# Kernel optimization log

Hardware: AMD Instinct MI355X
Metric: run time of the kernel (lower is better)

## Reference

```python
import jax, jax.numpy as jnp
import numpy as np
import math

D_MODEL = 1024
HEADS = 16
D_K = D_MODEL // HEADS
BATCH = 4
SEQ = 1024


def setup_inputs() -> dict:
    key = jax.random.key(0)
    ks = jax.random.split(key, 12)
    s = 1.0 / math.sqrt(D_MODEL)
    inp = {
        "q": jax.random.normal(ks[0], (BATCH, SEQ, D_MODEL), jnp.float32),
        "k": jax.random.normal(ks[1], (BATCH, SEQ, D_MODEL), jnp.float32),
        "v": jax.random.normal(ks[2], (BATCH, SEQ, D_MODEL), jnp.float32),
        # causal mask, broadcastable over (batch, heads)
        "mask": jnp.tril(jnp.ones((SEQ, SEQ), jnp.bool_))[None, None, :, :],
        "Wq": jax.random.normal(ks[3], (D_MODEL, D_MODEL), jnp.float32) * s,
        "bq": jax.random.normal(ks[4], (D_MODEL,), jnp.float32) * 0.01,
        "Wk": jax.random.normal(ks[5], (D_MODEL, D_MODEL), jnp.float32) * s,
        "bk": jax.random.normal(ks[6], (D_MODEL,), jnp.float32) * 0.01,
        "Wv": jax.random.normal(ks[7], (D_MODEL, D_MODEL), jnp.float32) * s,
        "bv": jax.random.normal(ks[8], (D_MODEL,), jnp.float32) * 0.01,
        "Wo": jax.random.normal(ks[9], (D_MODEL, D_MODEL), jnp.float32) * s,
        "bo": jax.random.normal(ks[10], (D_MODEL,), jnp.float32) * 0.01,
    }
    return inp


def reference(q, k, v, mask, Wq, bq, Wk, bk, Wv, bv, Wo, bo):
    B, S, _ = q.shape
    # projections (torch Linear: x @ W.T + b; here W stored as [in, out])
    def proj(x, W, b):
        return (x @ W + b).reshape(B, -1, HEADS, D_K).transpose(0, 2, 1, 3)

    Q = proj(q, Wq, bq)  # [B, H, S, Dk]
    K = proj(k, Wk, bk)
    V = proj(v, Wv, bv)

    scores = jnp.einsum("bhqd,bhkd->bhqk", Q, K) / math.sqrt(D_K)
    scores = jnp.where(mask, scores, jnp.float32(-1e9))
    attn = jax.nn.softmax(scores, axis=-1)  # dropout p=0.0 -> identity
    x = jnp.einsum("bhqk,bhkd->bhqd", attn, V)
    x = x.transpose(0, 2, 1, 3).reshape(B, S, D_MODEL)
    return x @ Wo + bo
```

## Files before the change

### kernel.cpp

```cpp
#include <hip/hip_runtime.h>
#include <math.h>

typedef __bf16 bf16_t;
typedef bf16_t bf16x8 __attribute__((ext_vector_type(8)));
typedef bf16_t bf16x4 __attribute__((ext_vector_type(4)));
typedef float  floatx4 __attribute__((ext_vector_type(4)));
typedef unsigned int u32;

#define MFMA_BF16(a, b, c) __builtin_amdgcn_mfma_f32_16x16x32_bf16((a), (b), (c), 0, 0, 0)

static constexpr int DMODEL = 1024;
static constexpr int NHEAD  = 16;
static constexpr int HDIM   = 64;
static constexpr int NBATCH = 4;
static constexpr int SEQLEN = 1024;
static constexpr int NTOK   = NBATCH * SEQLEN;

typedef __attribute__((address_space(3))) void       as3_void;
typedef __attribute__((address_space(1))) const void as1_cvoid;

__device__ __forceinline__ void gload16(const void* g, void* l) {
    __builtin_amdgcn_global_load_lds((as1_cvoid*)g, (as3_void*)l, 16, 0, 0);
}

__device__ __forceinline__ bf16x8 load_cvt8(const float* __restrict__ p) {
    floatx4 a = *(const floatx4*)p;
    floatx4 b = *(const floatx4*)(p + 4);
    bf16x8 r;
    r[0] = (bf16_t)a[0]; r[1] = (bf16_t)a[1]; r[2] = (bf16_t)a[2]; r[3] = (bf16_t)a[3];
    r[4] = (bf16_t)b[0]; r[5] = (bf16_t)b[1]; r[6] = (bf16_t)b[2]; r[7] = (bf16_t)b[3];
    return r;
}

__global__ __launch_bounds__(256) void prep(
    const float* __restrict__ W0, const float* __restrict__ W1,
    const float* __restrict__ W2, const float* __restrict__ W3,
    const float* __restrict__ q, const float* __restrict__ k, const float* __restrict__ v,
    bf16_t* __restrict__ Wt, bf16_t* __restrict__ Xr)
{
    __shared__ float tile[32][33];
    const int z = blockIdx.z;
    if (z < 4) {
        const float* W = (z == 0) ? W0 : (z == 1) ? W1 : (z == 2) ? W2 : W3;
        bf16_t* O = Wt + (size_t)z * DMODEL * DMODEL;
        const int tx = threadIdx.x & 31, ty = threadIdx.x >> 5;
        const int r0 = blockIdx.x * 32, c0 = blockIdx.y * 32;
#pragma unroll
        for (int i = 0; i < 32; i += 8)
            tile[ty + i][tx] = W[(size_t)(r0 + ty + i) * DMODEL + c0 + tx];
        __syncthreads();
#pragma unroll
        for (int i = 0; i < 32; i += 8)
            O[(size_t)(c0 + ty + i) * DMODEL + r0 + tx] = (bf16_t)tile[tx][ty + i];
    } else {
        const float* src = (z == 4) ? q : (z == 5) ? k : v;
        bf16_t* dst = Xr + (size_t)(z - 4) * ((size_t)NTOK * DMODEL);
        size_t i = (((size_t)blockIdx.y * 32 + blockIdx.x) * 256 + threadIdx.x) * 16;
        *(bf16x8*)(dst + i)     = load_cvt8(src + i);
        *(bf16x8*)(dst + i + 8) = load_cvt8(src + i + 8);
    }
}

__global__ __launch_bounds__(256) void transpose_w(
    const float* __restrict__ W0, const float* __restrict__ W1,
    const float* __restrict__ W2, const float* __restrict__ W3,
    bf16_t* __restrict__ out)
{
    __shared__ float tile[32][33];
    const float* W = (blockIdx.z == 0) ? W0 : (blockIdx.z == 1) ? W1
                   : (blockIdx.z == 2) ? W2 : W3;
    bf16_t* O = out + (size_t)blockIdx.z * DMODEL * DMODEL;
    int tx = threadIdx.x, ty = threadIdx.y;
    int r0 = blockIdx.x * 32, c0 = blockIdx.y * 32;
#pragma unroll
    for (int i = 0; i < 32; i += 8)
        tile[ty + i][tx] = W[(size_t)(r0 + ty + i) * DMODEL + c0 + tx];
    __syncthreads();
#pragma unroll
    for (int i = 0; i < 32; i += 8)
        O[(size_t)(c0 + ty + i) * DMODEL + r0 + tx] = (bf16_t)tile[tx][ty + i];
}
__global__ __launch_bounds__(256) void cvt_bf16(
    const float* __restrict__ src, bf16_t* __restrict__ dst)
{
    size_t i = ((size_t)blockIdx.x * 256 + threadIdx.x) * 8;
    *(bf16x8*)(dst + i) = load_cvt8(src + i);
}

__global__ __launch_bounds__(256) void gemm_qkv(
    const bf16_t* __restrict__ Xb, size_t astride, int mode0,
    const bf16_t* __restrict__ Wt,
    const float* __restrict__ bq, const float* __restrict__ bk, const float* __restrict__ bv,
    bf16_t* __restrict__ Qh, bf16_t* __restrict__ Kh, bf16_t* __restrict__ Vt)
{
    const int mode = mode0 + blockIdx.z;
    const bf16_t* A = Xb + astride * (size_t)blockIdx.z;
    const bf16_t* B = Wt + (size_t)mode * DMODEL * DMODEL;
    const float* bias = (mode == 0) ? bq : (mode == 1) ? bk : bv;
    bf16_t* out       = (mode == 0) ? Qh : (mode == 1) ? Kh : Vt;

    __shared__ __align__(16) bf16_t lA[2][128 * 32];
    __shared__ __align__(16) bf16_t lB[2][128 * 32];

    const int wave = threadIdx.x >> 6, lane = threadIdx.x & 63;
    const int quad = lane >> 4, l15 = lane & 15;
    const int wm = wave >> 1, wn = wave & 1;
    const int row0 = blockIdx.x * 128, col0 = blockIdx.y * 128;
    const int srow = lane >> 2, scol = (lane & 3) * 8;

    const floatx4 zero = {0.f, 0.f, 0.f, 0.f};
    floatx4 acc[4][4];
#pragma unroll
    for (int mt = 0; mt < 4; mt++)
#pragma unroll
        for (int nt = 0; nt < 4; nt++) acc[mt][nt] = zero;

#pragma unroll
    for (int j = 0; j < 2; j++) {
        const int seg = j * 4 + wave;
        gload16(A + (size_t)(row0 + seg * 16 + srow) * DMODEL + scol, lA[0] + seg * 512);
        gload16(B + (size_t)(col0 + seg * 16 + srow) * DMODEL + scol, lB[0] + seg * 512);
    }

    for (int it = 0; it < 32; it++) {
        __syncthreads();
        const int cur = it & 1;
        if (it + 1 < 32) {
            const int k1 = (it + 1) * 32;
            const int nb = cur ^ 1;
#pragma unroll
            for (int j = 0; j < 2; j++) {
                const int seg = j * 4 + wave;
                gload16(A + (size_t)(row0 + seg * 16 + srow) * DMODEL + k1 + scol, lA[nb] + seg * 512);
                gload16(B + (size_t)(col0 + seg * 16 + srow) * DMODEL + k1 + scol, lB[nb] + seg * 512);
            }
        }
        bf16x8 aF[4], bF[4];
#pragma unroll
        for (int t = 0; t < 4; t++) {
            aF[t] = *(const bf16x8*)(lA[cur] + (wm * 64 + t * 16 + l15) * 32 + quad * 8);
            bF[t] = *(const bf16x8*)(lB[cur] + (wn * 64 + t * 16 + l15) * 32 + quad * 8);
        }
#pragma unroll
        for (int mt = 0; mt < 4; mt++)
#pragma unroll
            for (int nt = 0; nt < 4; nt++)
                acc[mt][nt] = MFMA_BF16(aF[mt], bF[nt], acc[mt][nt]);
    }

#pragma unroll
    for (int nt = 0; nt < 4; nt++) {
        const int gn = col0 + wn * 64 + nt * 16 + l15;
        const float bb = bias[gn];
        const int hh = gn >> 6, dd = gn & 63;
#pragma unroll
        for (int mt = 0; mt < 4; mt++) {
#pragma unroll
            for (int r = 0; r < 4; r++) {
                const int tok = row0 + wm * 64 + mt * 16 + quad * 4 + r;
                const int b = tok >> 10, s = tok & 1023;
                float vv = acc[mt][nt][r] + bb;
                size_t addr;
                if (mode == 2) {
                    addr = ((size_t)((b * NHEAD + hh) * HDIM + dd)) * SEQLEN + s;
                } else {
                    if (mode == 0) vv *= 0.125f;
                    addr = ((size_t)((b * NHEAD + hh) * SEQLEN + s)) * HDIM + dd;
                }
                out[addr] = (bf16_t)vv;
            }
        }
    }
}

__global__ __launch_bounds__(256) void gemm_o(
    const bf16_t* __restrict__ Xa, const bf16_t* __restrict__ Wt,
    const float* __restrict__ bias, float* __restrict__ out)
{
    __shared__ __align__(16) bf16_t lA[2][64 * 32];
    __shared__ __align__(16) bf16_t lB[2][128 * 32];

    const int wave = threadIdx.x >> 6, lane = threadIdx.x & 63;
    const int quad = lane >> 4, l15 = lane & 15;
    const int wm = wave & 1, wn = wave >> 1;
    const int row0 = blockIdx.x * 64, col0 = blockIdx.y * 128;
    const int srow = lane >> 2, scol = (lane & 3) * 8;

    const floatx4 zero = {0.f, 0.f, 0.f, 0.f};
    floatx4 acc[2][4];
#pragma unroll
    for (int mt = 0; mt < 2; mt++)
#pragma unroll
        for (int nt = 0; nt < 4; nt++) acc[mt][nt] = zero;

    gload16(Xa + (size_t)(row0 + wave * 16 + srow) * DMODEL + scol, lA[0] + wave * 512);
#pragma unroll
    for (int j = 0; j < 2; j++) {
        const int seg = wave * 2 + j;
        gload16(Wt + (size_t)(col0 + seg * 16 + srow) * DMODEL + scol, lB[0] + seg * 512);
    }

    for (int it = 0; it < 32; it++) {
        __syncthreads();
        const int cur = it & 1;
        if (it + 1 < 32) {
            const int k1 = (it + 1) * 32;
            const int nb = cur ^ 1;
            gload16(Xa + (size_t)(row0 + wave * 16 + srow) * DMODEL + k1 + scol, lA[nb] + wave * 512);
#pragma unroll
            for (int j = 0; j < 2; j++) {
                const int seg = wave * 2 + j;
                gload16(Wt + (size_t)(col0 + seg * 16 + srow) * DMODEL + k1 + scol, lB[nb] + seg * 512);
            }
        }
        bf16x8 aF[2], bF[4];
#pragma unroll
        for (int t = 0; t < 2; t++)
            aF[t] = *(const bf16x8*)(lA[cur] + (wm * 32 + t * 16 + l15) * 32 + quad * 8);
#pragma unroll
        for (int t = 0; t < 4; t++)
            bF[t] = *(const bf16x8*)(lB[cur] + (wn * 64 + t * 16 + l15) * 32 + quad * 8);
#pragma unroll
        for (int mt = 0; mt < 2; mt++)
#pragma unroll
            for (int nt = 0; nt < 4; nt++)
                acc[mt][nt] = MFMA_BF16(aF[mt], bF[nt], acc[mt][nt]);
    }

#pragma unroll
    for (int nt = 0; nt < 4; nt++) {
        const int gn = col0 + wn * 64 + nt * 16 + l15;
        const float bb = bias[gn];
#pragma unroll
        for (int mt = 0; mt < 2; mt++) {
#pragma unroll
            for (int r = 0; r < 4; r++) {
                const int tok = row0 + wm * 32 + mt * 16 + quad * 4 + r;
                out[(size_t)tok * DMODEL + gn] = acc[mt][nt][r] + bb;
            }
        }
    }
}

#define LOAD_KV(S, KB) do {                                                            \
    const int kb_ = (KB);                                                              \
    _Pragma("unroll") for (int c = 0; c < 2; c++) {                                    \
        K0[S][c] = *(const bf16x8*)(Kp + (size_t)(kb_ + l15) * HDIM + c * 32 + quad * 8);      \
        K1[S][c] = *(const bf16x8*)(Kp + (size_t)(kb_ + 16 + l15) * HDIM + c * 32 + quad * 8); \
    }                                                                                  \
    _Pragma("unroll") for (int dt = 0; dt < 4; dt++)                                   \
        Vv[S][dt] = *(const bf16x8*)(Vp + (size_t)(dt * 16 + l15) * SEQLEN + kb_ + quad * 8);  \
} while (0)

#define SOFTMAX_PV(S0x, S1x, qbase, qrow, lacc, oacc) do {                             \
    const bool nomask = (kb + 31 <= (qbase));                                          \
    float ps = 0.f;                                                                    \
    union { bf16_t hh2[8]; u32 u[4]; } pk;                                             \
    _Pragma("unroll") for (int r = 0; r < 4; r++) {                                    \
        const int key0 = kb + quad * 4 + r;                                            \
        float s0 = (nomask || key0 <= (qrow))      ? S0x[r] : -1e30f;                  \
        float s1 = (nomask || key0 + 16 <= (qrow)) ? S1x[r] : -1e30f;                  \
        float e0 = __expf(s0), e1 = __expf(s1);                                        \
        ps += e0 + e1;                                                                 \
        pk.hh2[r] = (bf16_t)e0; pk.hh2[4 + r] = (bf16_t)e1;                            \
    }                                                                                  \
    lacc += ps;                                                                        \
    u32 a0 = __shfl(pk.u[0], srcA), a1 = __shfl(pk.u[1], srcA);                        \
    u32 a2 = __shfl(pk.u[0], srcB), a3 = __shfl(pk.u[1], srcB);                        \
    u32 b0 = __shfl(pk.u[2], srcA), b1 = __shfl(pk.u[3], srcA);                        \
    u32 b2 = __shfl(pk.u[2], srcB), b3 = __shfl(pk.u[3], srcB);                        \
    union { u32 u[4]; bf16x8 v; } bP;                                                  \
    bP.u[0] = hiP ? b0 : a0; bP.u[1] = hiP ? b1 : a1;                                  \
    bP.u[2] = hiP ? b2 : a2; bP.u[3] = hiP ? b3 : a3;                                  \
    _Pragma("unroll") for (int dt = 0; dt < 4; dt++)                                   \
        oacc[dt] = MFMA_BF16(Vv[SET][dt], bP.v, oacc[dt]);                             \
} while (0)

#define ATTN_STEP(KC, SETC) do {                                                       \
    const int SET = (SETC);                                                            \
    const int kb = (KC) * 32;                                                          \
    const bool doA = ((KC) < nkA);                                                     \
    floatx4 S0B = zero, S1B = zero, S0A = zero, S1A = zero;                            \
    _Pragma("unroll") for (int c = 0; c < 2; c++) {                                    \
        S0B = MFMA_BF16(K0[SET][c], bQB[c], S0B);                                      \
        S1B = MFMA_BF16(K1[SET][c], bQB[c], S1B);                                      \
    }                                                                                  \
    if (doA) {                                                                         \
        _Pragma("unroll") for (int c = 0; c < 2; c++) {                                \
            S0A = MFMA_BF16(K0[SET][c], bQA[c], S0A);                                  \
            S1A = MFMA_BF16(K1[SET][c], bQA[c], S1A);                                  \
        }                                                                              \
    }                                                                                  \
    SOFTMAX_PV(S0B, S1B, qbaseB, qrowB, lB_, oB);                                      \
    if (doA) { SOFTMAX_PV(S0A, S1A, qbaseA, qrowA, lA_, oA); }                         \
} while (0)

__global__ __launch_bounds__(256, 2) void attn(
    const bf16_t* __restrict__ Qh, const bf16_t* __restrict__ Kh,
    const bf16_t* __restrict__ Vt, bf16_t* __restrict__ X)
{
    const int wave = threadIdx.x >> 6, lane = threadIdx.x & 63;
    const int quad = lane >> 4, l15 = lane & 15;
    const int L = blockIdx.x;
    const int bh = (L & 7) * 8 + ((L >> 3) & 7);
    const int pb = L >> 6;
    const int t  = pb * 4 + wave;
    const int b = bh >> 4, h = bh & 15;

    const int qbaseA = 16 * t, qbaseB = 1008 - 16 * t;
    const int qrowA = qbaseA + l15, qrowB = qbaseB + l15;
    const int nkA = t / 2 + 1, nkB = 32 - t / 2;

    const bf16_t* Qp = Qh + (size_t)bh * SEQLEN * HDIM;
    const bf16_t* Kp = Kh + (size_t)bh * SEQLEN * HDIM;
    const bf16_t* Vp = Vt + (size_t)bh * HDIM * SEQLEN;

    bf16x8 bQA[2], bQB[2];
#pragma unroll
    for (int c = 0; c < 2; c++) {
        bQA[c] = *(const bf16x8*)(Qp + (size_t)qrowA * HDIM + c * 32 + quad * 8);
        bQB[c] = *(const bf16x8*)(Qp + (size_t)qrowB * HDIM + c * 32 + quad * 8);
    }

    const floatx4 zero = {0.f, 0.f, 0.f, 0.f};
    float lA_ = 0.f, lB_ = 0.f;
    floatx4 oA[4], oB[4];
#pragma unroll
    for (int dt = 0; dt < 4; dt++) { oA[dt] = zero; oB[dt] = zero; }

    const int srcA = ((quad & 1) ? 32 : 0) + l15;
    const int srcB = srcA + 16;
    const bool hiP = (quad >= 2);

    bf16x8 K0[2][2], K1[2][2], Vv[2][4];
    LOAD_KV(0, 0);

    for (int kc = 0; kc < nkB; kc += 2) {
        if (kc + 1 < nkB) LOAD_KV(1, (kc + 1) * 32);
        ATTN_STEP(kc, 0);
        if (kc + 1 < nkB) {
            if (kc + 2 < nkB) LOAD_KV(0, (kc + 2) * 32);
            ATTN_STEP(kc + 1, 1);
        }
    }

    lA_ += __shfl_xor(lA_, 16); lA_ += __shfl_xor(lA_, 32);
    lB_ += __shfl_xor(lB_, 16); lB_ += __shfl_xor(lB_, 32);

    const float invA = 1.f / lA_, invB = 1.f / lB_;
#pragma unroll
    for (int dt = 0; dt < 4; dt++) {
        bf16x4 va, vb;
#pragma unroll
        for (int r = 0; r < 4; r++) {
            va[r] = (bf16_t)(oA[dt][r] * invA);
            vb[r] = (bf16_t)(oB[dt][r] * invB);
        }
        const size_t cofs = (size_t)h * HDIM + dt * 16 + quad * 4;
        *(bf16x4*)(&X[((size_t)(b * SEQLEN + qrowA)) * DMODEL + cofs]) = va;
        *(bf16x4*)(&X[((size_t)(b * SEQLEN + qrowB)) * DMODEL + cofs]) = vb;
    }
}

extern "C" void kernel_launch(void* const* d_in, const int* in_sizes, int n_in,
                              void* d_out, int out_size, void* d_ws, size_t ws_size,
                              hipStream_t stream)
{
    const float* q  = (const float*)d_in[0];
    const float* k  = (const float*)d_in[1];
    const float* v  = (const float*)d_in[2];
    const float* Wq = (const float*)d_in[4];
    const float* bq = (const float*)d_in[5];
    const float* Wk = (const float*)d_in[6];
    const float* bk = (const float*)d_in[7];
    const float* Wv = (const float*)d_in[8];
    const float* bv = (const float*)d_in[9];
    const float* Wo = (const float*)d_in[10];
    const float* bo = (const float*)d_in[11];
    float* out = (float*)d_out;

    char* ws = (char*)d_ws;
    const size_t MB = 1ull << 20;
    const size_t NELEM = (size_t)NTOK * DMODEL;
    bf16_t* Wt = (bf16_t*)ws;
    bf16_t* Qh = (bf16_t*)(ws + 8 * MB);
    bf16_t* Kh = (bf16_t*)(ws + 16 * MB);
    bf16_t* Vt = (bf16_t*)(ws + 24 * MB);
    bf16_t* Xr = (bf16_t*)(ws + 32 * MB);

    if (ws_size >= 56 * MB) {
        prep<<<dim3(32, 32, 7), dim3(256), 0, stream>>>(Wq, Wk, Wv, Wo, q, k, v, Wt, Xr);
        gemm_qkv<<<dim3(32, 8, 3), dim3(256), 0, stream>>>(
            Xr, NELEM, 0, Wt, bq, bk, bv, Qh, Kh, Vt);
    } else {
        transpose_w<<<dim3(32, 32, 4), dim3(32, 8), 0, stream>>>(Wq, Wk, Wv, Wo, Wt);
        const float* qkv_in[3] = {q, k, v};
        for (int m = 0; m < 3; m++) {
            cvt_bf16<<<dim3(2048), dim3(256), 0, stream>>>(qkv_in[m], Xr);
            gemm_qkv<<<dim3(32, 8, 1), dim3(256), 0, stream>>>(
                Xr, 0, m, Wt, bq, bk, bv, Qh, Kh, Vt);
        }
    }

    bf16_t* Xa = Xr;
    attn<<<dim3(512), dim3(256), 0, stream>>>(Qh, Kh, Vt, Xa);
    gemm_o<<<dim3(64, 8), dim3(256), 0, stream>>>(
        Xa, Wt + 3 * (size_t)DMODEL * DMODEL, bo, out);
}
```

Before: 238.3 us.

## Split attention key loop across wave pairs and combine partials via LDS

```diff
diff --git a/kernel.cpp b/kernel.cpp
--- a/kernel.cpp
+++ b/kernel.cpp
@@ -241,16 +241,6 @@
         }
     }
 }
-
-#define LOAD_KV(S, KB) do {                                                            \
-    const int kb_ = (KB);                                                              \
-    _Pragma("unroll") for (int c = 0; c < 2; c++) {                                    \
-        K0[S][c] = *(const bf16x8*)(Kp + (size_t)(kb_ + l15) * HDIM + c * 32 + quad * 8);      \
-        K1[S][c] = *(const bf16x8*)(Kp + (size_t)(kb_ + 16 + l15) * HDIM + c * 32 + quad * 8); \
-    }                                                                                  \
-    _Pragma("unroll") for (int dt = 0; dt < 4; dt++)                                   \
-        Vv[S][dt] = *(const bf16x8*)(Vp + (size_t)(dt * 16 + l15) * SEQLEN + kb_ + quad * 8);  \
-} while (0)
 
 #define SOFTMAX_PV(S0x, S1x, qbase, qrow, lacc, oacc) do {                             \
     const bool nomask = (kb + 31 <= (qbase));                                          \
@@ -273,38 +263,21 @@
     bP.u[0] = hiP ? b0 : a0; bP.u[1] = hiP ? b1 : a1;                                  \
     bP.u[2] = hiP ? b2 : a2; bP.u[3] = hiP ? b3 : a3;                                  \
     _Pragma("unroll") for (int dt = 0; dt < 4; dt++)                                   \
-        oacc[dt] = MFMA_BF16(Vv[SET][dt], bP.v, oacc[dt]);                             \
+        oacc[dt] = MFMA_BF16(Vv[dt], bP.v, oacc[dt]);                                  \
 } while (0)
 
-#define ATTN_STEP(KC, SETC) do {                                                       \
-    const int SET = (SETC);                                                            \
-    const int kb = (KC) * 32;                                                          \
-    const bool doA = ((KC) < nkA);                                                     \
-    floatx4 S0B = zero, S1B = zero, S0A = zero, S1A = zero;                            \
-    _Pragma("unroll") for (int c = 0; c < 2; c++) {                                    \
-        S0B = MFMA_BF16(K0[SET][c], bQB[c], S0B);                                      \
-        S1B = MFMA_BF16(K1[SET][c], bQB[c], S1B);                                      \
-    }                                                                                  \
-    if (doA) {                                                                         \
-        _Pragma("unroll") for (int c = 0; c < 2; c++) {                                \
-            S0A = MFMA_BF16(K0[SET][c], bQA[c], S0A);                                  \
-            S1A = MFMA_BF16(K1[SET][c], bQA[c], S1A);                                  \
-        }                                                                              \
-    }                                                                                  \
-    SOFTMAX_PV(S0B, S1B, qbaseB, qrowB, lB_, oB);                                      \
-    if (doA) { SOFTMAX_PV(S0A, S1A, qbaseA, qrowA, lA_, oA); }                         \
-} while (0)
-
-__global__ __launch_bounds__(256, 2) void attn(
+__global__ __launch_bounds__(256, 4) void attn(
     const bf16_t* __restrict__ Qh, const bf16_t* __restrict__ Kh,
     const bf16_t* __restrict__ Vt, bf16_t* __restrict__ X)
 {
+    __shared__ __align__(8) float comb[2][64][34];
     const int wave = threadIdx.x >> 6, lane = threadIdx.x & 63;
     const int quad = lane >> 4, l15 = lane & 15;
     const int L = blockIdx.x;
     const int bh = (L & 7) * 8 + ((L >> 3) & 7);
-    const int pb = L >> 6;
-    const int t  = pb * 4 + wave;
+    const int pb2 = L >> 6;
+    const int t   = pb2 * 2 + (wave >> 1);
+    const int half = wave & 1;
     const int b = bh >> 4, h = bh & 15;
 
     const int qbaseA = 16 * t, qbaseB = 1008 - 16 * t;
@@ -332,33 +305,77 @@
     const int srcB = srcA + 16;
     const bool hiP = (quad >= 2);
 
-    bf16x8 K0[2][2], K1[2][2], Vv[2][4];
-    LOAD_KV(0, 0);
-
-    for (int kc = 0; kc < nkB; kc += 2) {
-        if (kc + 1 < nkB) LOAD_KV(1, (kc + 1) * 32);
-        ATTN_STEP(kc, 0);
-        if (kc + 1 < nkB) {
-            if (kc + 2 < nkB) LOAD_KV(0, (kc + 2) * 32);
-            ATTN_STEP(kc + 1, 1);
-        }
-    }
-
-    lA_ += __shfl_xor(lA_, 16); lA_ += __shfl_xor(lA_, 32);
-    lB_ += __shfl_xor(lB_, 16); lB_ += __shfl_xor(lB_, 32);
-
-    const float invA = 1.f / lA_, invB = 1.f / lB_;
-#pragma unroll
-    for (int dt = 0; dt < 4; dt++) {
-        bf16x4 va, vb;
-#pragma unroll
-        for (int r = 0; r < 4; r++) {
-            va[r] = (bf16_t)(oA[dt][r] * invA);
-            vb[r] = (bf16_t)(oB[dt][r] * invB);
-        }
-        const size_t cofs = (size_t)h * HDIM + dt * 16 + quad * 4;
-        *(bf16x4*)(&X[((size_t)(b * SEQLEN + qrowA)) * DMODEL + cofs]) = va;
-        *(bf16x4*)(&X[((size_t)(b * SEQLEN + qrowB)) * DMODEL + cofs]) = vb;
+    for (int kc = half; kc < nkB; kc += 2) {
+        const int kb = kc * 32;
+        bf16x8 K0[2], K1[2], Vv[4];
+#pragma unroll
+        for (int c = 0; c < 2; c++) {
+            K0[c] = *(const bf16x8*)(Kp + (size_t)(kb + l15) * HDIM + c * 32 + quad * 8);
+            K1[c] = *(const bf16x8*)(Kp + (size_t)(kb + 16 + l15) * HDIM + c * 32 + quad * 8);
+        }
+#pragma unroll
+        for (int dt = 0; dt < 4; dt++)
+            Vv[dt] = *(const bf16x8*)(Vp + (size_t)(dt * 16 + l15) * SEQLEN + kb + quad * 8);
+
+        const bool doA = (kc < nkA);
+        floatx4 S0B = zero, S1B = zero, S0A = zero, S1A = zero;
+#pragma unroll
+        for (int c = 0; c < 2; c++) {
+            S0B = MFMA_BF16(K0[c], bQB[c], S0B);
+            S1B = MFMA_BF16(K1[c], bQB[c], S1B);
+        }
+        if (doA) {
+#pragma unroll
+            for (int c = 0; c < 2; c++) {
+                S0A = MFMA_BF16(K0[c], bQA[c], S0A);
+                S1A = MFMA_BF16(K1[c], bQA[c], S1A);
+            }
+        }
+        SOFTMAX_PV(S0B, S1B, qbaseB, qrowB, lB_, oB);
+        if (doA) { SOFTMAX_PV(S0A, S1A, qbaseA, qrowA, lA_, oA); }
+    }
+
+    const int pr = wave >> 1;
+    if (half) {
+        float2* d2 = (float2*)&comb[pr][lane][0];
+#pragma unroll
+        for (int dt = 0; dt < 4; dt++) {
+            d2[2 * dt]     = make_float2(oA[dt][0], oA[dt][1]);
+            d2[2 * dt + 1] = make_float2(oA[dt][2], oA[dt][3]);
+            d2[8 + 2 * dt]     = make_float2(oB[dt][0], oB[dt][1]);
+            d2[8 + 2 * dt + 1] = make_float2(oB[dt][2], oB[dt][3]);
+        }
+        d2[16] = make_float2(lA_, lB_);
+    }
+    __syncthreads();
+    if (!half) {
+        const float2* s2 = (const float2*)&comb[pr][lane][0];
+#pragma unroll
+        for (int dt = 0; dt < 4; dt++) {
+            float2 x0 = s2[2 * dt], x1 = s2[2 * dt + 1];
+            float2 y0 = s2[8 + 2 * dt], y1 = s2[8 + 2 * dt + 1];
+            oA[dt][0] += x0.x; oA[dt][1] += x0.y; oA[dt][2] += x1.x; oA[dt][3] += x1.y;
+            oB[dt][0] += y0.x; oB[dt][1] += y0.y; oB[dt][2] += y1.x; oB[dt][3] += y1.y;
+        }
+        float2 lp = s2[16];
+        lA_ += lp.x; lB_ += lp.y;
+
+        lA_ += __shfl_xor(lA_, 16); lA_ += __shfl_xor(lA_, 32);
+        lB_ += __shfl_xor(lB_, 16); lB_ += __shfl_xor(lB_, 32);
+
+        const float invA = 1.f / lA_, invB = 1.f / lB_;
+#pragma unroll
+        for (int dt = 0; dt < 4; dt++) {
+            bf16x4 va, vb;
+#pragma unroll
+            for (int r = 0; r < 4; r++) {
+                va[r] = (bf16_t)(oA[dt][r] * invA);
+                vb[r] = (bf16_t)(oB[dt][r] * invB);
+            }
+            const size_t cofs = (size_t)h * HDIM + dt * 16 + quad * 4;
+            *(bf16x4*)(&X[((size_t)(b * SEQLEN + qrowA)) * DMODEL + cofs]) = va;
+            *(bf16x4*)(&X[((size_t)(b * SEQLEN + qrowB)) * DMODEL + cofs]) = vb;
+        }
     }
 }
 
@@ -403,7 +420,7 @@
     }
 
     bf16_t* Xa = Xr;
-    attn<<<dim3(512), dim3(256), 0, stream>>>(Qh, Kh, Vt, Xa);
+    attn<<<dim3(1024), dim3(256), 0, stream>>>(Qh, Kh, Vt, Xa);
     gemm_o<<<dim3(64, 8), dim3(256), 0, stream>>>(
         Xa, Wt + 3 * (size_t)DMODEL * DMODEL, bo, out);
 }
```

Measured after the change: 235.6 us. About the same (-1.1%).
